# Kernel tuning notes

Measured on AMD Instinct MI355X. Metric: run time of the kernel, lower is better.

The kernel has to match this reference:

```python
import jax, jax.numpy as jnp
import numpy as np

B, N, D, H, DG = 1, 1024, 512, 8, 64
DK = D // H
EPS = 1e-5


def _layer_norm(x, g, b):
    m = jnp.mean(x, axis=-1, keepdims=True)
    v = jnp.var(x, axis=-1, keepdims=True)
    return (x - m) / jnp.sqrt(v + EPS) * g + b


def _box_rel_embedding(box):
    # box: (B, N, 4) = x_min, y_min, x_max, y_max
    x_min, y_min, x_max, y_max = [box[..., i] for i in range(4)]  # each (B, N)
    cx = (x_min + x_max) * 0.5
    cy = (y_min + y_max) * 0.5
    w = x_max - x_min + 1.0
    h = y_max - y_min + 1.0
    dx = jnp.log(jnp.clip(jnp.abs((cx[:, :, None] - cx[:, None, :]) / w[:, :, None]), 0.001))
    dy = jnp.log(jnp.clip(jnp.abs((cy[:, :, None] - cy[:, None, :]) / h[:, :, None]), 0.001))
    dw = jnp.log(w[:, :, None] / w[:, None, :])
    dh = jnp.log(h[:, :, None] / h[:, None, :])
    pos = jnp.stack([dx, dy, dw, dh], axis=-1)  # (B, N, N, 4)
    dim_mat = 1.0 / jnp.power(1000.0, jnp.arange(DG // 8, dtype=jnp.float32) / (DG // 8))  # (8,)
    mul = (100.0 * pos[..., None] * dim_mat).reshape(pos.shape[0], pos.shape[1], pos.shape[2], -1)  # (B,N,N,32)
    return jnp.concatenate([jnp.sin(mul), jnp.cos(mul)], axis=-1)  # (B, N, N, 64)


def _split_heads(x, W, b):
    # torch permute(2,0,1,3).view(-1, len, d_k): head-major flattening
    return (x @ W.T + b).reshape(B, N, H, DK).transpose(2, 0, 1, 3).reshape(H * B, N, DK)


def _forward(input_query, input_key, input_value, input_box,
             Wq, bq, Wk, bk, Wv, bv, Wo, bo, WG_w, WG_b,
             ln0_g, ln0_b, ln_g, ln_b):
    residual = input_query
    emb = _box_rel_embedding(input_box)  # (B, N, N, 64)
    # per-head linear (64 -> 1) then relu: (B, H, N, N)
    w_g = jax.nn.relu(jnp.einsum('bijg,hg->bhij', emb, WG_w) + WG_b[None, :, None, None])
    q = _split_heads(input_query, Wq, bq)  # (H*B, N, DK)
    k = _split_heads(input_key, Wk, bk)
    v = _split_heads(input_value, Wv, bv)
    scores = jnp.einsum('xnd,xmd->xnm', q, k) / np.sqrt(DK).astype(np.float32)  # (H*B, N, N)
    # original adds (B,H,N,N) to (H*B,N,N): only valid for B==1
    w_mn = jax.nn.softmax(jnp.log(jnp.clip(w_g.reshape(H * B, N, N), 1e-6)) + scores, axis=-1)
    x = jnp.einsum('xnm,xmd->xnd', w_mn, v)  # (H*B, N, DK)
    # faithful to original: transpose(1,2) then view(nbatches, -1, h*d_k)
    x = x.transpose(0, 2, 1).reshape(B, -1, H * DK)  # (B, N, D)
    out0 = _layer_norm(x + residual, ln0_g, ln0_b)
    out = out0 @ Wo.T + bo  # dropout = identity (eval mode)
    return _layer_norm(out + out0, ln_g, ln_b)


def setup_inputs() -> dict:
    key = jax.random.key(0)
    ks = jax.random.split(key, 12)
    inp = {}
    inp['input_query'] = jax.random.normal(ks[0], (B, N, D), dtype=jnp.float32)
    inp['input_key'] = jax.random.normal(ks[1], (B, N, D), dtype=jnp.float32)
    inp['input_value'] = jax.random.normal(ks[2], (B, N, D), dtype=jnp.float32)
    mins = jax.random.uniform(ks[3], (B, N, 2), dtype=jnp.float32) * 500.0
    sizes = jax.random.uniform(ks[4], (B, N, 2), dtype=jnp.float32) * 99.0 + 1.0
    inp['input_box'] = jnp.concatenate([mins, mins + sizes], axis=-1)  # valid boxes
    s = 0.02
    inp['Wq'] = jax.random.normal(ks[5], (D, D), dtype=jnp.float32) * s
    inp['bq'] = jnp.zeros((D,), dtype=jnp.float32)
    inp['Wk'] = jax.random.normal(ks[6], (D, D), dtype=jnp.float32) * s
    inp['bk'] = jnp.zeros((D,), dtype=jnp.float32)
    inp['Wv'] = jax.random.normal(ks[7], (D, D), dtype=jnp.float32) * s
    inp['bv'] = jnp.zeros((D,), dtype=jnp.float32)
    inp['Wo'] = jax.random.normal(ks[8], (D, D), dtype=jnp.float32) * s
    inp['bo'] = jnp.zeros((D,), dtype=jnp.float32)
    inp['WG_w'] = jax.random.normal(ks[9], (H, DG), dtype=jnp.float32) * 0.1
    inp['WG_b'] = jax.random.normal(ks[10], (H,), dtype=jnp.float32) * 0.1
    inp['ln0_g'] = jnp.ones((D,), dtype=jnp.float32)
    inp['ln0_b'] = jnp.zeros((D,), dtype=jnp.float32)
    inp['ln_g'] = jnp.ones((D,), dtype=jnp.float32)
    inp['ln_b'] = jnp.zeros((D,), dtype=jnp.float32)
    return inp


def reference(input_query, input_key, input_value, input_box,
              Wq, bq, Wk, bk, Wv, bv, Wo, bo, WG_w, WG_b,
              ln0_g, ln0_b, ln_g, ln_b):
    return _forward(input_query, input_key, input_value, input_box,
                    Wq, bq, Wk, bk, Wv, bv, Wo, bo, WG_w, WG_b,
                    ln0_g, ln0_b, ln_g, ln_b)
```

## Files before the change

### kernel.cpp

```cpp
#include <hip/hip_runtime.h>
#include <cstddef>

#define NTOK 1024
#define DMODEL 512
#define NHEAD 8
#define DKH 64
#define NSPLIT 4
#define JQ 256

typedef __attribute__((ext_vector_type(4))) float f32x4;
typedef __attribute__((ext_vector_type(8))) __bf16 bf16x8;
typedef __attribute__((ext_vector_type(4))) __bf16 bf16x4;
typedef __attribute__((ext_vector_type(4))) unsigned short u16x4;
typedef __attribute__((ext_vector_type(8))) unsigned short u16x8;
typedef __attribute__((ext_vector_type(4))) _Float16 f16x4;
typedef unsigned short ushort_t;

__device__ __forceinline__ float wave_sum_f(float v){
  #pragma unroll
  for (int m=1; m<64; m<<=1) v += __shfl_xor(v, m, 64);
  return v;
}
__device__ __forceinline__ unsigned short f2bf(float f){
  __bf16 b = (__bf16)f;
  return __builtin_bit_cast(unsigned short, b);
}
__device__ __forceinline__ float bf2f(unsigned short u){
  return (float)__builtin_bit_cast(__bf16, u);
}

__device__ __forceinline__ float fract_hw(float x){
  float r; asm("v_fract_f32 %0, %1" : "=v"(r) : "v"(x)); return r;
}
__device__ __forceinline__ float sin_rev(float rev){
  float f = fract_hw(rev);
  float s; asm("v_sin_f32 %0, %1" : "=v"(s) : "v"(f)); return s;
}
__device__ __forceinline__ float cos_rev(float rev){
  float f = fract_hw(rev);
  float c; asm("v_cos_f32 %0, %1" : "=v"(c) : "v"(f)); return c;
}
__device__ __forceinline__ float log_hw(float x){
  float l; asm("v_log_f32 %0, %1" : "=v"(l) : "v"(x));
  return 0.69314718056f * l;
}
__device__ __forceinline__ float exp_hw(float x){
  float y = x * 1.44269504f;
  float e; asm("v_exp_f32 %0, %1" : "=v"(e) : "v"(y));
  return e;
}

__global__ __launch_bounds__(256) void k_pre(
    const float* __restrict__ box, const float* __restrict__ WGw, const float* __restrict__ WGb,
    _Float16* __restrict__ wg16,
    const float* __restrict__ q, const float* __restrict__ k, const float* __restrict__ v,
    const float* __restrict__ wq, const float* __restrict__ wk, const float* __restrict__ wv,
    const float* __restrict__ wo,
    ushort_t* __restrict__ qb, ushort_t* __restrict__ kb, ushort_t* __restrict__ vb,
    ushort_t* __restrict__ wqb, ushort_t* __restrict__ wkb, ushort_t* __restrict__ wvb,
    ushort_t* __restrict__ wob){
  const int t = threadIdx.x;
  if (blockIdx.x >= 1024){
    int gi = (blockIdx.x - 1024)*256 + t;
    const float* s; ushort_t* d; int off;
    if (gi < 196608){
      int seg = gi >> 16;
      off = (gi & 65535)*8;
      s = seg==0 ? q : seg==1 ? k : v;
      d = seg==0 ? qb : seg==1 ? kb : vb;
    } else {
      int g2 = gi - 196608;
      int seg = g2 >> 15;
      off = (g2 & 32767)*8;
      s = seg==0 ? wq : seg==1 ? wk : seg==2 ? wv : wo;
      d = seg==0 ? wqb : seg==1 ? wkb : seg==2 ? wvb : wob;
    }
    float4 a = *(const float4*)(s + off);
    float4 b = *(const float4*)(s + off + 4);
    u16x4 o0, o1;
    o0[0]=f2bf(a.x); o0[1]=f2bf(a.y); o0[2]=f2bf(a.z); o0[3]=f2bf(a.w);
    o1[0]=f2bf(b.x); o1[1]=f2bf(b.y); o1[2]=f2bf(b.z); o1[3]=f2bf(b.w);
    *(u16x4*)(d + off) = o0;
    *(u16x4*)(d + off + 4) = o1;
    return;
  }
  __shared__ float arr[4][1024];
  #pragma unroll
  for (int u=0; u<4; u++){
    int idx = u*256 + t;
    float4 b4 = *(const float4*)(box + idx*4);
    arr[0][idx] = (b4.x + b4.z)*0.5f;
    arr[1][idx] = (b4.y + b4.w)*0.5f;
    arr[2][idx] = log_hw(b4.z - b4.x + 1.0f);
    arr[3][idx] = log_hw(b4.w - b4.y + 1.0f);
  }
  const int i = blockIdx.x;
  const int lane = t & 63, w = t >> 6, li = lane & 15, g = lane >> 4;
  float4 bi = *(const float4*)(box + i*4);
  float wi = bi.z - bi.x + 1.0f, hi = bi.w - bi.y + 1.0f;
  float Pi = (g==0) ? (bi.x+bi.z)*0.5f : (g==1) ? (bi.y+bi.w)*0.5f
           : (g==2) ? log_hw(wi) : log_hw(hi);
  float Ri = (g==0) ? 1.0f/wi : (g==1) ? 1.0f/hi : 1.0f;
  const bool doLog = (g < 2);
  bf16x8 wfs = {}, wfc = {};
  float wgb_li = 0.0f;
  if (li < 8){
    #pragma unroll
    for (int e=0; e<8; e++){
      wfs[e] = (__bf16)WGw[li*64 + g*8 + e];
      wfc[e] = (__bf16)WGw[li*64 + 32 + g*8 + e];
    }
    wgb_li = WGb[li];
  }
  __syncthreads();
  const float* parr = &arr[g][0];
  const float DMrev[8] = {15.9154943f, 6.7115094f, 2.8302196f, 1.1934938f,
                          0.5032921f, 0.2122365f, 0.08949941f, 0.0377416f};
  const int jbeg = w*256;
  for (int it=0; it<16; ++it){
    int j = jbeg + it*16 + li;
    float diff = (Pi - parr[j])*Ri;
    float lg = log_hw(fmaxf(fabsf(diff), 1e-3f));
    float dv = doLog ? lg : diff;
    bf16x8 afs, afc;
    #pragma unroll
    for (int e=0; e<8; e++){
      float rev = dv * DMrev[e];
      afs[e] = (__bf16)sin_rev(rev);
      afc[e] = (__bf16)cos_rev(rev);
    }
    f32x4 acc = (f32x4){0.f,0.f,0.f,0.f};
    acc = __builtin_amdgcn_mfma_f32_16x16x32_bf16(afs, wfs, acc, 0,0,0);
    acc = __builtin_amdgcn_mfma_f32_16x16x32_bf16(afc, wfc, acc, 0,0,0);
    if (li < 8){
      f16x4 o;
      #pragma unroll
      for (int r=0; r<4; r++)
        o[r] = (_Float16)fmaxf(acc[r] + wgb_li, 6.103515625e-05f);
      *(f16x4*)(wg16 + (((size_t)li<<20) + ((size_t)i<<10) + jbeg + it*16 + g*4)) = o;
    }
  }
}

__global__ __launch_bounds__(128) void k_mm_qkv(
    const ushort_t* __restrict__ Aq, const ushort_t* __restrict__ Ak, const ushort_t* __restrict__ Av,
    const ushort_t* __restrict__ Wqb, const ushort_t* __restrict__ Wkb, const ushort_t* __restrict__ Wvb,
    const float* __restrict__ bq, const float* __restrict__ bk, const float* __restrict__ bv,
    ushort_t* __restrict__ Qb, ushort_t* __restrict__ Kb, ushort_t* __restrict__ Vt){
  const int z = blockIdx.z;
  const ushort_t* A = z==0 ? Aq : z==1 ? Ak : Av;
  const ushort_t* W = z==0 ? Wqb : z==1 ? Wkb : Wvb;
  const float* bias = z==0 ? bq : z==1 ? bk : bv;
  const int t = threadIdx.x, lane = t & 63, w = t >> 6;
  const int li = lane & 15, g = lane >> 4;
  const int m0 = blockIdx.y*32;
  const int n0 = blockIdx.x*64 + w*32;
  const ushort_t* ar = A + (size_t)(m0+li)*DMODEL + g*8;
  const ushort_t* wr = W + (size_t)(n0+li)*DMODEL + g*8;
  f32x4 acc[2][2] = {};
  if (z < 2){
    #pragma unroll
    for (int k0=0; k0<DMODEL; k0+=64){
      bf16x8 wf0a = *(const bf16x8*)(wr + k0);
      bf16x8 wf0b = *(const bf16x8*)(wr + k0 + 32);
      bf16x8 wf1a = *(const bf16x8*)(wr + 16*DMODEL + k0);
      bf16x8 wf1b = *(const bf16x8*)(wr + 16*DMODEL + k0 + 32);
      bf16x8 af0a = *(const bf16x8*)(ar + k0);
      bf16x8 af0b = *(const bf16x8*)(ar + k0 + 32);
      bf16x8 af1a = *(const bf16x8*)(ar + 16*DMODEL + k0);
      bf16x8 af1b = *(const bf16x8*)(ar + 16*DMODEL + k0 + 32);
      acc[0][0] = __builtin_amdgcn_mfma_f32_16x16x32_bf16(wf0a, af0a, acc[0][0], 0,0,0);
      acc[0][0] = __builtin_amdgcn_mfma_f32_16x16x32_bf16(wf0b, af0b, acc[0][0], 0,0,0);
      acc[0][1] = __builtin_amdgcn_mfma_f32_16x16x32_bf16(wf0a, af1a, acc[0][1], 0,0,0);
      acc[0][1] = __builtin_amdgcn_mfma_f32_16x16x32_bf16(wf0b, af1b, acc[0][1], 0,0,0);
      acc[1][0] = __builtin_amdgcn_mfma_f32_16x16x32_bf16(wf1a, af0a, acc[1][0], 0,0,0);
      acc[1][0] = __builtin_amdgcn_mfma_f32_16x16x32_bf16(wf1b, af0b, acc[1][0], 0,0,0);
      acc[1][1] = __builtin_amdgcn_mfma_f32_16x16x32_bf16(wf1a, af1a, acc[1][1], 0,0,0);
      acc[1][1] = __builtin_amdgcn_mfma_f32_16x16x32_bf16(wf1b, af1b, acc[1][1], 0,0,0);
    }
    ushort_t* C = z ? Kb : Qb;
    #pragma unroll
    for (int nf=0; nf<2; nf++){
      int n = n0 + nf*16 + g*4;
      float4 b4 = *(const float4*)(bias + n);
      const float* bp = (const float*)&b4;
      #pragma unroll
      for (int mf=0; mf<2; mf++){
        int m = m0 + mf*16 + li;
        u16x4 o;
        #pragma unroll
        for (int r=0; r<4; r++) o[r] = f2bf(acc[nf][mf][r] + bp[r]);
        *(u16x4*)(C + (size_t)m*DMODEL + n) = o;
      }
    }
  } else {
    #pragma unroll
    for (int k0=0; k0<DMODEL; k0+=64){
      bf16x8 wf0a = *(const bf16x8*)(wr + k0);
      bf16x8 wf0b = *(const bf16x8*)(wr + k0 + 32);
      bf16x8 wf1a = *(const bf16x8*)(wr + 16*DMODEL + k0);
      bf16x8 wf1b = *(const bf16x8*)(wr + 16*DMODEL + k0 + 32);
      bf16x8 af0a = *(const bf16x8*)(ar + k0);
      bf16x8 af0b = *(const bf16x8*)(ar + k0 + 32);
      bf16x8 af1a = *(const bf16x8*)(ar + 16*DMODEL + k0);
      bf16x8 af1b = *(const bf16x8*)(ar + 16*DMODEL + k0 + 32);
      acc[0][0] = __builtin_amdgcn_mfma_f32_16x16x32_bf16(af0a, wf0a, acc[0][0], 0,0,0);
      acc[0][0] = __builtin_amdgcn_mfma_f32_16x16x32_bf16(af0b, wf0b, acc[0][0], 0,0,0);
      acc[0][1] = __builtin_amdgcn_mfma_f32_16x16x32_bf16(af0a, wf1a, acc[0][1], 0,0,0);
      acc[0][1] = __builtin_amdgcn_mfma_f32_16x16x32_bf16(af0b, wf1b, acc[0][1], 0,0,0);
      acc[1][0] = __builtin_amdgcn_mfma_f32_16x16x32_bf16(af1a, wf0a, acc[1][0], 0,0,0);
      acc[1][0] = __builtin_amdgcn_mfma_f32_16x16x32_bf16(af1b, wf0b, acc[1][0], 0,0,0);
      acc[1][1] = __builtin_amdgcn_mfma_f32_16x16x32_bf16(af1a, wf1a, acc[1][1], 0,0,0);
      acc[1][1] = __builtin_amdgcn_mfma_f32_16x16x32_bf16(af1b, wf1b, acc[1][1], 0,0,0);
    }
    #pragma unroll
    for (int mf=0; mf<2; mf++){
      int m = m0 + mf*16 + g*4;
      #pragma unroll
      for (int nf=0; nf<2; nf++){
        int n = n0 + nf*16 + li;
        float bn = bias[n];
        u16x4 o;
        #pragma unroll
        for (int r=0; r<4; r++) o[r] = f2bf(acc[mf][nf][r] + bn);
        *(u16x4*)(Vt + (((size_t)(n>>6))<<16) + ((size_t)(n&63)<<10) + m) = o;
      }
    }
  }
}

__global__ __launch_bounds__(512) void k_attn3(const ushort_t* __restrict__ Qb,
     const ushort_t* __restrict__ Kb, const ushort_t* __restrict__ Vt,
     const _Float16* __restrict__ wg, ushort_t* __restrict__ Xpt, float* __restrict__ rsp){
  __shared__ ushort_t Ks[256*68];
  __shared__ ushort_t Vs[64*264];
  const int t = threadIdx.x;
  const int itg = blockIdx.x, h = blockIdx.y, sp = blockIdx.z;
  const int jbeg = sp*JQ;
  {
    const int r = t >> 3, c = (t & 7)*8;
    #pragma unroll
    for (int p=0; p<4; p++){
      u16x8 kv = *(const u16x8*)(Kb + (size_t)(jbeg + p*64 + r)*DMODEL + h*DKH + c);
      *(u16x8*)(Ks + (p*64 + r)*68 + c) = kv;
      u16x8 vv = *(const u16x8*)(Vt + ((size_t)h<<16) + (size_t)r*NTOK + jbeg + p*64 + c);
      *(u16x8*)(Vs + r*264 + p*64 + c) = vv;
    }
  }
  const int lane = t & 63, w = t >> 6;
  const int i0 = (itg*8 + w)*16;
  const int li = lane & 15, g = lane >> 4;
  const ushort_t* qp = Qb + (size_t)(i0+li)*DMODEL + h*DKH + g*8;
  bf16x8 qf0 = *(const bf16x8*)(qp);
  bf16x8 qf1 = *(const bf16x8*)(qp + 32);
  const _Float16* gbase = wg + ((size_t)h<<20) + ((size_t)(i0+li)<<10) + jbeg + g*4;
  f32x4 xacc[4];
  #pragma unroll
  for (int mf=0; mf<4; mf++) xacc[mf] = (f32x4){0.f,0.f,0.f,0.f};
  float rsum = 0.f;
  __syncthreads();
  #pragma unroll
  for (int jj = 0; jj < JQ; jj += 32){
    const ushort_t* kp = Ks + (jj + li)*68 + g*8;
    bf16x8 a00 = *(const bf16x8*)(kp);
    bf16x8 a01 = *(const bf16x8*)(kp + 32);
    bf16x8 a10 = *(const bf16x8*)(kp + 16*68);
    bf16x8 a11 = *(const bf16x8*)(kp + 16*68 + 32);
    f32x4 s0 = (f32x4){0.f,0.f,0.f,0.f};
    f32x4 s1 = (f32x4){0.f,0.f,0.f,0.f};
    s0 = __builtin_amdgcn_mfma_f32_16x16x32_bf16(a00, qf0, s0, 0,0,0);
    s0 = __builtin_amdgcn_mfma_f32_16x16x32_bf16(a01, qf1, s0, 0,0,0);
    s1 = __builtin_amdgcn_mfma_f32_16x16x32_bf16(a10, qf0, s1, 0,0,0);
    s1 = __builtin_amdgcn_mfma_f32_16x16x32_bf16(a11, qf1, s1, 0,0,0);
    f16x4 g0 = *(const f16x4*)(gbase + jj);
    f16x4 g1 = *(const f16x4*)(gbase + jj + 16);
    float p[8];
    #pragma unroll
    for (int r=0; r<4; r++){ p[r]   = (float)g0[r] * exp_hw(s0[r]*0.125f); rsum += p[r]; }
    #pragma unroll
    for (int r=0; r<4; r++){ p[4+r] = (float)g1[r] * exp_hw(s1[r]*0.125f); rsum += p[4+r]; }
    bf16x8 pb;
    pb[0]=(__bf16)p[0]; pb[1]=(__bf16)p[1]; pb[2]=(__bf16)p[2]; pb[3]=(__bf16)p[3];
    pb[4]=(__bf16)p[4]; pb[5]=(__bf16)p[5]; pb[6]=(__bf16)p[6]; pb[7]=(__bf16)p[7];
    #pragma unroll
    for (int mf=0; mf<4; mf++){
      const ushort_t* vp = Vs + (size_t)(li + mf*16)*264 + jj + g*4;
      bf16x4 lo = *(const bf16x4*)(vp);
      bf16x4 hi = *(const bf16x4*)(vp + 16);
      bf16x8 vf = __builtin_shufflevector(lo, hi, 0,1,2,3,4,5,6,7);
      xacc[mf] = __builtin_amdgcn_mfma_f32_16x16x32_bf16(vf, pb, xacc[mf], 0,0,0);
    }
  }
  rsum += __shfl_xor(rsum, 16, 64);
  rsum += __shfl_xor(rsum, 32, 64);
  if (lane < 16) rsp[((size_t)sp*NHEAD + h)*NTOK + i0 + li] = rsum;
  __syncthreads();
  float* xw = (float*)Ks + w*(16*68);
  #pragma unroll
  for (int mf=0; mf<4; mf++)
    *(f32x4*)&xw[li*68 + mf*16 + g*4] = xacc[mf];
  __builtin_amdgcn_s_waitcnt(0);
  float xv[16];
  #pragma unroll
  for (int r=0; r<16; r++) xv[r] = xw[r*68 + lane];
  u16x8 o0, o1;
  #pragma unroll
  for (int r=0; r<8; r++){ o0[r] = f2bf(xv[r]); o1[r] = f2bf(xv[8+r]); }
  ushort_t* xp = Xpt + (((size_t)sp*NHEAD + h)*DKH + lane)*NTOK + i0;
  *(u16x8*)(xp)     = o0;
  *(u16x8*)(xp + 8) = o1;
}

__global__ __launch_bounds__(256) void k_ln0c(const ushort_t* __restrict__ Xpt,
        const float* __restrict__ rsp, const float* __restrict__ resid,
        const float* __restrict__ g, const float* __restrict__ b,
        float* __restrict__ out0, ushort_t* __restrict__ out0b){
  const int n = blockIdx.x, t = threadIdx.x;
  const int h = n >> 7, dk = (n >> 1) & 63, mo = (n & 1)*512;
  const int i0 = mo + t, i1 = mo + t + 256;
  float s0v=0.f, s1v=0.f, r0=0.f, r1=0.f;
  #pragma unroll
  for (int sp=0; sp<NSPLIT; sp++){
    const ushort_t* base = Xpt + (((size_t)sp*NHEAD + h)*DKH + dk)*NTOK;
    s0v += bf2f(base[i0]);
    s1v += bf2f(base[i1]);
    const float* rb = rsp + ((size_t)sp*NHEAD + h)*NTOK;
    r0 += rb[i0];
    r1 += rb[i1];
  }
  float x0 = s0v/r0 + resid[(size_t)n*DMODEL + t];
  float x1 = s1v/r1 + resid[(size_t)n*DMODEL + t + 256];
  __shared__ float red[8];
  float s = wave_sum_f(x0 + x1);
  float q = wave_sum_f(x0*x0 + x1*x1);
  int wid = t >> 6, lane = t & 63;
  if (lane == 0){ red[wid] = s; red[4+wid] = q; }
  __syncthreads();
  float S = red[0]+red[1]+red[2]+red[3];
  float Q = red[4]+red[5]+red[6]+red[7];
  float mean = S * (1.0f/512.0f);
  float var = Q * (1.0f/512.0f) - mean*mean;
  float rs = rsqrtf(var + 1e-5f);
  float y0 = (x0-mean)*rs*g[t] + b[t];
  float y1 = (x1-mean)*rs*g[t+256] + b[t+256];
  out0[(size_t)n*DMODEL + t]        = y0;
  out0[(size_t)n*DMODEL + t + 256]  = y1;
  out0b[(size_t)n*DMODEL + t]       = f2bf(y0);
  out0b[(size_t)n*DMODEL + t + 256] = f2bf(y1);
}

__global__ __launch_bounds__(512) void k_mm_o_ln(
    const ushort_t* __restrict__ A, const ushort_t* __restrict__ W,
    const float* __restrict__ bo, const float* __restrict__ add,
    const float* __restrict__ lng, const float* __restrict__ lnb, float* __restrict__ out){
  const int t = threadIdx.x, lane = t & 63, w = t >> 6;
  const int li = lane & 15, g = lane >> 4;
  const int m0 = blockIdx.x*16;
  const int n0 = w*64;
  const ushort_t* ar = A + (size_t)(m0+li)*DMODEL + g*8;
  const ushort_t* wr = W + (size_t)(n0+li)*DMODEL + g*8;
  f32x4 acc[4] = {};
  #pragma unroll
  for (int k0=0; k0<DMODEL; k0+=64){
    bf16x8 afa = *(const bf16x8*)(ar + k0);
    bf16x8 afb = *(const bf16x8*)(ar + k0 + 32);
    #pragma unroll
    for (int nf=0; nf<4; nf++){
      const ushort_t* wp = wr + (size_t)nf*16*DMODEL + k0;
      bf16x8 wfa = *(const bf16x8*)(wp);
      bf16x8 wfb = *(const bf16x8*)(wp + 32);
      acc[nf] = __builtin_amdgcn_mfma_f32_16x16x32_bf16(wfa, afa, acc[nf], 0,0,0);
      acc[nf] = __builtin_amdgcn_mfma_f32_16x16x32_bf16(wfb, afb, acc[nf], 0,0,0);
    }
  }
  const int m = m0 + li;
  float s = 0.f, qq = 0.f;
  f32x4 v[4];
  #pragma unroll
  for (int nf=0; nf<4; nf++){
    int n = n0 + nf*16 + g*4;
    f32x4 b4 = *(const f32x4*)(bo + n);
    f32x4 a4 = *(const f32x4*)(add + (size_t)m*DMODEL + n);
    #pragma unroll
    for (int r=0; r<4; r++){
      float x = acc[nf][r] + b4[r] + a4[r];
      v[nf][r] = x; s += x; qq += x*x;
    }
  }
  s  += __shfl_xor(s, 16, 64);  s  += __shfl_xor(s, 32, 64);
  qq += __shfl_xor(qq, 16, 64); qq += __shfl_xor(qq, 32, 64);
  __shared__ float red[8][16][2];
  if (g == 0){ red[w][li][0] = s; red[w][li][1] = qq; }
  __syncthreads();
  float S = 0.f, Q = 0.f;
  #pragma unroll
  for (int u=0; u<8; u++){ S += red[u][li][0]; Q += red[u][li][1]; }
  float mean = S * (1.0f/512.0f);
  float var = Q * (1.0f/512.0f) - mean*mean;
  float rs = rsqrtf(var + 1e-5f);
  #pragma unroll
  for (int nf=0; nf<4; nf++){
    int n = n0 + nf*16 + g*4;
    f32x4 g4 = *(const f32x4*)(lng + n);
    f32x4 be = *(const f32x4*)(lnb + n);
    f32x4 o;
    #pragma unroll
    for (int r=0; r<4; r++) o[r] = (v[nf][r]-mean)*rs*g4[r] + be[r];
    *(f32x4*)(out + (size_t)m*DMODEL + n) = o;
  }
}

extern "C" void kernel_launch(void* const* d_in, const int* in_sizes, int n_in,
                              void* d_out, int out_size, void* d_ws, size_t ws_size,
                              hipStream_t stream){
  (void)in_sizes; (void)n_in; (void)out_size; (void)ws_size;
  const float* in_q = (const float*)d_in[0];
  const float* in_k = (const float*)d_in[1];
  const float* in_v = (const float*)d_in[2];
  const float* box  = (const float*)d_in[3];
  const float* Wq   = (const float*)d_in[4];
  const float* bq   = (const float*)d_in[5];
  const float* Wk   = (const float*)d_in[6];
  const float* bk   = (const float*)d_in[7];
  const float* Wv   = (const float*)d_in[8];
  const float* bv   = (const float*)d_in[9];
  const float* Wo   = (const float*)d_in[10];
  const float* bo   = (const float*)d_in[11];
  const float* WGw  = (const float*)d_in[12];
  const float* WGb  = (const float*)d_in[13];
  const float* ln0g = (const float*)d_in[14];
  const float* ln0b = (const float*)d_in[15];
  const float* lng  = (const float*)d_in[16];
  const float* lnb  = (const float*)d_in[17];

  float* ws = (float*)d_ws;
  ushort_t* Abq  = (ushort_t*)(ws + 0);
  ushort_t* Abk  = (ushort_t*)(ws + 262144);
  ushort_t* Abv  = (ushort_t*)(ws + 524288);
  ushort_t* Wqb  = (ushort_t*)(ws + 786432);
  ushort_t* Wkb  = (ushort_t*)(ws + 917504);
  ushort_t* Wvb  = (ushort_t*)(ws + 1048576);
  ushort_t* Wob  = (ushort_t*)(ws + 1179648);
  ushort_t* Qb   = (ushort_t*)(ws + 1310720);
  ushort_t* Kb   = (ushort_t*)(ws + 1572864);
  ushort_t* Vt   = (ushort_t*)(ws + 1835008);
  _Float16* wg16 = (_Float16*)(ws + 2097152);
  ushort_t* Xpt  = (ushort_t*)(ws + 6291456);
  float*    rsp  = ws + 8388608;
  float*    out0 = ws + 8421376;
  ushort_t* out0b= (ushort_t*)(ws + 8945664);
  float*    out  = (float*)d_out;

  k_pre<<<dim3(2304), dim3(256), 0, stream>>>(box, WGw, WGb, wg16,
            in_q, in_k, in_v, Wq, Wk, Wv, Wo,
            Abq, Abk, Abv, Wqb, Wkb, Wvb, Wob);
  k_mm_qkv<<<dim3(8,32,3), dim3(128), 0, stream>>>(Abq, Abk, Abv, Wqb, Wkb, Wvb,
            bq, bk, bv, Qb, Kb, Vt);
  k_attn3<<<dim3(8,8,4), dim3(512), 0, stream>>>(Qb, Kb, Vt, wg16, Xpt, rsp);
  k_ln0c<<<dim3(1024), dim3(256), 0, stream>>>(Xpt, rsp, in_q, ln0g, ln0b, out0, out0b);
  k_mm_o_ln<<<dim3(64), dim3(512), 0, stream>>>(out0b, Wob, bo, out0, lng, lnb, out);
}
```

Measured before the change: 77.92 us.

## Fuse all five stages into one persistent kernel with grid-wide barriers

Replaces the five separate launches (preprocessing, QKV projection, attention, LayerNorm-combine, output projection with LayerNorm) with one persistent kernel of 256 blocks of 512 threads. A software grid barrier built on global atomics separates the stages, and the barrier counter is reset with a memset before each launch. The aim is to remove per-launch overhead and the gaps between kernels. In exchange, every stage now runs on a fixed 256-block grid whose work distribution differs from the original tuned grids. The barrier also relies on all blocks being co-resident, so it can deadlock or add spin cost if they are not.

After: 222.7 us. 2.86x slower.

```diff
diff --git a/kernel.cpp b/kernel.cpp
--- a/kernel.cpp
+++ b/kernel.cpp
@@ -50,363 +50,385 @@
   return e;
 }
 
-__global__ __launch_bounds__(256) void k_pre(
+__device__ __forceinline__ void gsync(unsigned* bar){
+  __syncthreads();
+  if (threadIdx.x == 0){
+    unsigned gen = __hip_atomic_load(bar+1, __ATOMIC_RELAXED, __HIP_MEMORY_SCOPE_AGENT);
+    unsigned prev = __hip_atomic_fetch_add(bar, 1u, __ATOMIC_ACQ_REL, __HIP_MEMORY_SCOPE_AGENT);
+    if (prev == 255u){
+      __hip_atomic_store(bar, 0u, __ATOMIC_RELAXED, __HIP_MEMORY_SCOPE_AGENT);
+      __hip_atomic_store(bar+1, gen+1u, __ATOMIC_RELEASE, __HIP_MEMORY_SCOPE_AGENT);
+    } else {
+      while (__hip_atomic_load(bar+1, __ATOMIC_ACQUIRE, __HIP_MEMORY_SCOPE_AGENT) == gen)
+        __builtin_amdgcn_s_sleep(2);
+    }
+  }
+  __syncthreads();
+}
+
+__global__ __launch_bounds__(512) void k_mega(
     const float* __restrict__ box, const float* __restrict__ WGw, const float* __restrict__ WGb,
     _Float16* __restrict__ wg16,
-    const float* __restrict__ q, const float* __restrict__ k, const float* __restrict__ v,
-    const float* __restrict__ wq, const float* __restrict__ wk, const float* __restrict__ wv,
-    const float* __restrict__ wo,
-    ushort_t* __restrict__ qb, ushort_t* __restrict__ kb, ushort_t* __restrict__ vb,
-    ushort_t* __restrict__ wqb, ushort_t* __restrict__ wkb, ushort_t* __restrict__ wvb,
-    ushort_t* __restrict__ wob){
+    const float* __restrict__ inq, const float* __restrict__ ink, const float* __restrict__ inv,
+    const float* __restrict__ Wq, const float* __restrict__ Wk, const float* __restrict__ Wv,
+    const float* __restrict__ Wo,
+    ushort_t* __restrict__ Abq, ushort_t* __restrict__ Abk, ushort_t* __restrict__ Abv,
+    ushort_t* __restrict__ Wqb, ushort_t* __restrict__ Wkb, ushort_t* __restrict__ Wvb,
+    ushort_t* __restrict__ Wob,
+    const float* __restrict__ bq, const float* __restrict__ bk, const float* __restrict__ bv,
+    ushort_t* __restrict__ Qb, ushort_t* __restrict__ Kb, ushort_t* __restrict__ Vt,
+    ushort_t* __restrict__ Xpt, float* __restrict__ rsp,
+    const float* __restrict__ ln0g, const float* __restrict__ ln0b,
+    float* __restrict__ out0, ushort_t* __restrict__ out0b,
+    const float* __restrict__ bo, const float* __restrict__ lng, const float* __restrict__ lnb,
+    float* __restrict__ out, unsigned* bar){
+  __shared__ __align__(16) char smem[68608];
   const int t = threadIdx.x;
-  if (blockIdx.x >= 1024){
-    int gi = (blockIdx.x - 1024)*256 + t;
-    const float* s; ushort_t* d; int off;
-    if (gi < 196608){
-      int seg = gi >> 16;
-      off = (gi & 65535)*8;
-      s = seg==0 ? q : seg==1 ? k : v;
-      d = seg==0 ? qb : seg==1 ? kb : vb;
+  const int b = blockIdx.x;
+  const int lane = t & 63, w = t >> 6;
+  const int li = lane & 15, g = lane >> 4;
+  const int wid = b*8 + w;
+
+  {
+    float* arr = (float*)smem;
+    #pragma unroll
+    for (int u=0; u<2; u++){
+      int idx = u*512 + t;
+      float4 b4 = *(const float4*)(box + idx*4);
+      arr[idx]      = (b4.x + b4.z)*0.5f;
+      arr[1024+idx] = (b4.y + b4.w)*0.5f;
+      arr[2048+idx] = log_hw(b4.z - b4.x + 1.0f);
+      arr[3072+idx] = log_hw(b4.w - b4.y + 1.0f);
+    }
+    __syncthreads();
+    bf16x8 wfs = {}, wfc = {};
+    float wgb_li = 0.0f;
+    if (li < 8){
+      #pragma unroll
+      for (int e=0; e<8; e++){
+        wfs[e] = (__bf16)WGw[li*64 + g*8 + e];
+        wfc[e] = (__bf16)WGw[li*64 + 32 + g*8 + e];
+      }
+      wgb_li = WGb[li];
+    }
+    const float* parr = arr + g*1024;
+    const float DMrev[8] = {15.9154943f, 6.7115094f, 2.8302196f, 1.1934938f,
+                            0.5032921f, 0.2122365f, 0.08949941f, 0.0377416f};
+    #pragma unroll
+    for (int pass=0; pass<2; pass++){
+      const int unit = wid + pass*2048;
+      const int i = unit >> 2;
+      const int jbeg = (unit & 3)*256;
+      float4 bi = *(const float4*)(box + i*4);
+      float wi_ = bi.z - bi.x + 1.0f, hi_ = bi.w - bi.y + 1.0f;
+      float Pi = (g==0) ? (bi.x+bi.z)*0.5f : (g==1) ? (bi.y+bi.w)*0.5f
+               : (g==2) ? log_hw(wi_) : log_hw(hi_);
+      float Ri = (g==0) ? 1.0f/wi_ : (g==1) ? 1.0f/hi_ : 1.0f;
+      const bool doLog = (g < 2);
+      for (int it=0; it<16; ++it){
+        int j = jbeg + it*16 + li;
+        float diff = (Pi - parr[j])*Ri;
+        float lg = log_hw(fmaxf(fabsf(diff), 1e-3f));
+        float dv = doLog ? lg : diff;
+        bf16x8 afs, afc;
+        #pragma unroll
+        for (int e=0; e<8; e++){
+          float rev = dv * DMrev[e];
+          afs[e] = (__bf16)sin_rev(rev);
+          afc[e] = (__bf16)cos_rev(rev);
+        }
+        f32x4 acc = (f32x4){0.f,0.f,0.f,0.f};
+        acc = __builtin_amdgcn_mfma_f32_16x16x32_bf16(afs, wfs, acc, 0,0,0);
+        acc = __builtin_amdgcn_mfma_f32_16x16x32_bf16(afc, wfc, acc, 0,0,0);
+        if (li < 8){
+          f16x4 o;
+          #pragma unroll
+          for (int r=0; r<4; r++)
+            o[r] = (_Float16)fmaxf(acc[r] + wgb_li, 6.103515625e-05f);
+          *(f16x4*)(wg16 + (((size_t)li<<20) + ((size_t)i<<10) + jbeg + it*16 + g*4)) = o;
+        }
+      }
+    }
+    #pragma unroll
+    for (int kk=0; kk<3; kk++){
+      int gi = b*512 + t + kk*131072;
+      if (gi < 327680){
+        const float* s; ushort_t* d; int off;
+        if (gi < 196608){
+          int seg = gi >> 16;
+          off = (gi & 65535)*8;
+          s = seg==0 ? inq : seg==1 ? ink : inv;
+          d = seg==0 ? Abq : seg==1 ? Abk : Abv;
+        } else {
+          int g2 = gi - 196608;
+          int seg = g2 >> 15;
+          off = (g2 & 32767)*8;
+          s = seg==0 ? Wq : seg==1 ? Wk : seg==2 ? Wv : Wo;
+          d = seg==0 ? Wqb : seg==1 ? Wkb : seg==2 ? Wvb : Wob;
+        }
+        float4 a = *(const float4*)(s + off);
+        float4 b4 = *(const float4*)(s + off + 4);
+        u16x4 o0, o1;
+        o0[0]=f2bf(a.x); o0[1]=f2bf(a.y); o0[2]=f2bf(a.z); o0[3]=f2bf(a.w);
+        o1[0]=f2bf(b4.x); o1[1]=f2bf(b4.y); o1[2]=f2bf(b4.z); o1[3]=f2bf(b4.w);
+        *(u16x4*)(d + off) = o0;
+        *(u16x4*)(d + off + 4) = o1;
+      }
+    }
+  }
+  gsync(bar);
+
+  if (wid < 1536){
+    const int z = wid / 512;
+    const int rem = wid - z*512;
+    const int my = rem >> 4;
+    const int nx = (rem & 15) >> 1;
+    const int w2 = rem & 1;
+    const int m0 = my*32;
+    const int n0 = nx*64 + w2*32;
+    const ushort_t* A = z==0 ? Abq : z==1 ? Abk : Abv;
+    const ushort_t* W = z==0 ? Wqb : z==1 ? Wkb : Wvb;
+    const float* bias = z==0 ? bq : z==1 ? bk : bv;
+    const ushort_t* ar = A + (size_t)(m0+li)*DMODEL + g*8;
+    const ushort_t* wr = W + (size_t)(n0+li)*DMODEL + g*8;
+    f32x4 acc[2][2] = {};
+    if (z < 2){
+      #pragma unroll
+      for (int k0=0; k0<DMODEL; k0+=64){
+        bf16x8 wf0a = *(const bf16x8*)(wr + k0);
+        bf16x8 wf0b = *(const bf16x8*)(wr + k0 + 32);
+        bf16x8 wf1a = *(const bf16x8*)(wr + 16*DMODEL + k0);
+        bf16x8 wf1b = *(const bf16x8*)(wr + 16*DMODEL + k0 + 32);
+        bf16x8 af0a = *(const bf16x8*)(ar + k0);
+        bf16x8 af0b = *(const bf16x8*)(ar + k0 + 32);
+        bf16x8 af1a = *(const bf16x8*)(ar + 16*DMODEL + k0);
+        bf16x8 af1b = *(const bf16x8*)(ar + 16*DMODEL + k0 + 32);
+        acc[0][0] = __builtin_amdgcn_mfma_f32_16x16x32_bf16(wf0a, af0a, acc[0][0], 0,0,0);
+        acc[0][0] = __builtin_amdgcn_mfma_f32_16x16x32_bf16(wf0b, af0b, acc[0][0], 0,0,0);
+        acc[0][1] = __builtin_amdgcn_mfma_f32_16x16x32_bf16(wf0a, af1a, acc[0][1], 0,0,0);
+        acc[0][1] = __builtin_amdgcn_mfma_f32_16x16x32_bf16(wf0b, af1b, acc[0][1], 0,0,0);
+        acc[1][0] = __builtin_amdgcn_mfma_f32_16x16x32_bf16(wf1a, af0a, acc[1][0], 0,0,0);
+        acc[1][0] = __builtin_amdgcn_mfma_f32_16x16x32_bf16(wf1b, af0b, acc[1][0], 0,0,0);
+        acc[1][1] = __builtin_amdgcn_mfma_f32_16x16x32_bf16(wf1a, af1a, acc[1][1], 0,0,0);
+        acc[1][1] = __builtin_amdgcn_mfma_f32_16x16x32_bf16(wf1b, af1b, acc[1][1], 0,0,0);
+      }
+      ushort_t* C = z ? Kb : Qb;
+      #pragma unroll
+      for (int nf=0; nf<2; nf++){
+        int n = n0 + nf*16 + g*4;
+        float4 b4 = *(const float4*)(bias + n);
+        const float* bp = (const float*)&b4;
+        #pragma unroll
+        for (int mf=0; mf<2; mf++){
+          int m = m0 + mf*16 + li;
+          u16x4 o;
+          #pragma unroll
+          for (int r=0; r<4; r++) o[r] = f2bf(acc[nf][mf][r] + bp[r]);
+          *(u16x4*)(C + (size_t)m*DMODEL + n) = o;
+        }
+      }
     } else {
-      int g2 = gi - 196608;
-      int seg = g2 >> 15;
-      off = (g2 & 32767)*8;
-      s = seg==0 ? wq : seg==1 ? wk : seg==2 ? wv : wo;
-      d = seg==0 ? wqb : seg==1 ? wkb : seg==2 ? wvb : wob;
-    }
-    float4 a = *(const float4*)(s + off);
-    float4 b = *(const float4*)(s + off + 4);
-    u16x4 o0, o1;
-    o0[0]=f2bf(a.x); o0[1]=f2bf(a.y); o0[2]=f2bf(a.z); o0[3]=f2bf(a.w);
-    o1[0]=f2bf(b.x); o1[1]=f2bf(b.y); o1[2]=f2bf(b.z); o1[3]=f2bf(b.w);
-    *(u16x4*)(d + off) = o0;
-    *(u16x4*)(d + off + 4) = o1;
-    return;
-  }
-  __shared__ float arr[4][1024];
-  #pragma unroll
-  for (int u=0; u<4; u++){
-    int idx = u*256 + t;
-    float4 b4 = *(const float4*)(box + idx*4);
-    arr[0][idx] = (b4.x + b4.z)*0.5f;
-    arr[1][idx] = (b4.y + b4.w)*0.5f;
-    arr[2][idx] = log_hw(b4.z - b4.x + 1.0f);
-    arr[3][idx] = log_hw(b4.w - b4.y + 1.0f);
-  }
-  const int i = blockIdx.x;
-  const int lane = t & 63, w = t >> 6, li = lane & 15, g = lane >> 4;
-  float4 bi = *(const float4*)(box + i*4);
-  float wi = bi.z - bi.x + 1.0f, hi = bi.w - bi.y + 1.0f;
-  float Pi = (g==0) ? (bi.x+bi.z)*0.5f : (g==1) ? (bi.y+bi.w)*0.5f
-           : (g==2) ? log_hw(wi) : log_hw(hi);
-  float Ri = (g==0) ? 1.0f/wi : (g==1) ? 1.0f/hi : 1.0f;
-  const bool doLog = (g < 2);
-  bf16x8 wfs = {}, wfc = {};
-  float wgb_li = 0.0f;
-  if (li < 8){
-    #pragma unroll
-    for (int e=0; e<8; e++){
-      wfs[e] = (__bf16)WGw[li*64 + g*8 + e];
-      wfc[e] = (__bf16)WGw[li*64 + 32 + g*8 + e];
-    }
-    wgb_li = WGb[li];
-  }
-  __syncthreads();
-  const float* parr = &arr[g][0];
-  const float DMrev[8] = {15.9154943f, 6.7115094f, 2.8302196f, 1.1934938f,
-                          0.5032921f, 0.2122365f, 0.08949941f, 0.0377416f};
-  const int jbeg = w*256;
-  for (int it=0; it<16; ++it){
-    int j = jbeg + it*16 + li;
-    float diff = (Pi - parr[j])*Ri;
-    float lg = log_hw(fmaxf(fabsf(diff), 1e-3f));
-    float dv = doLog ? lg : diff;
-    bf16x8 afs, afc;
-    #pragma unroll
-    for (int e=0; e<8; e++){
-      float rev = dv * DMrev[e];
-      afs[e] = (__bf16)sin_rev(rev);
-      afc[e] = (__bf16)cos_rev(rev);
-    }
-    f32x4 acc = (f32x4){0.f,0.f,0.f,0.f};
-    acc = __builtin_amdgcn_mfma_f32_16x16x32_bf16(afs, wfs, acc, 0,0,0);
-    acc = __builtin_amdgcn_mfma_f32_16x16x32_bf16(afc, wfc, acc, 0,0,0);
-    if (li < 8){
-      f16x4 o;
-      #pragma unroll
-      for (int r=0; r<4; r++)
-        o[r] = (_Float16)fmaxf(acc[r] + wgb_li, 6.103515625e-05f);
-      *(f16x4*)(wg16 + (((size_t)li<<20) + ((size_t)i<<10) + jbeg + it*16 + g*4)) = o;
-    }
-  }
-}
-
-__global__ __launch_bounds__(128) void k_mm_qkv(
-    const ushort_t* __restrict__ Aq, const ushort_t* __restrict__ Ak, const ushort_t* __restrict__ Av,
-    const ushort_t* __restrict__ Wqb, const ushort_t* __restrict__ Wkb, const ushort_t* __restrict__ Wvb,
-    const float* __restrict__ bq, const float* __restrict__ bk, const float* __restrict__ bv,
-    ushort_t* __restrict__ Qb, ushort_t* __restrict__ Kb, ushort_t* __restrict__ Vt){
-  const int z = blockIdx.z;
-  const ushort_t* A = z==0 ? Aq : z==1 ? Ak : Av;
-  const ushort_t* W = z==0 ? Wqb : z==1 ? Wkb : Wvb;
-  const float* bias = z==0 ? bq : z==1 ? bk : bv;
-  const int t = threadIdx.x, lane = t & 63, w = t >> 6;
-  const int li = lane & 15, g = lane >> 4;
-  const int m0 = blockIdx.y*32;
-  const int n0 = blockIdx.x*64 + w*32;
-  const ushort_t* ar = A + (size_t)(m0+li)*DMODEL + g*8;
-  const ushort_t* wr = W + (size_t)(n0+li)*DMODEL + g*8;
-  f32x4 acc[2][2] = {};
-  if (z < 2){
+      #pragma unroll
+      for (int k0=0; k0<DMODEL; k0+=64){
+        bf16x8 wf0a = *(const bf16x8*)(wr + k0);
+        bf16x8 wf0b = *(const bf16x8*)(wr + k0 + 32);
+        bf16x8 wf1a = *(const bf16x8*)(wr + 16*DMODEL + k0);
+        bf16x8 wf1b = *(const bf16x8*)(wr + 16*DMODEL + k0 + 32);
+        bf16x8 af0a = *(const bf16x8*)(ar + k0);
+        bf16x8 af0b = *(const bf16x8*)(ar + k0 + 32);
+        bf16x8 af1a = *(const bf16x8*)(ar + 16*DMODEL + k0);
+        bf16x8 af1b = *(const bf16x8*)(ar + 16*DMODEL + k0 + 32);
+        acc[0][0] = __builtin_amdgcn_mfma_f32_16x16x32_bf16(af0a, wf0a, acc[0][0], 0,0,0);
+        acc[0][0] = __builtin_amdgcn_mfma_f32_16x16x32_bf16(af0b, wf0b, acc[0][0], 0,0,0);
+        acc[0][1] = __builtin_amdgcn_mfma_f32_16x16x32_bf16(af0a, wf1a, acc[0][1], 0,0,0);
+        acc[0][1] = __builtin_amdgcn_mfma_f32_16x16x32_bf16(af0b, wf1b, acc[0][1], 0,0,0);
+        acc[1][0] = __builtin_amdgcn_mfma_f32_16x16x32_bf16(af1a, wf0a, acc[1][0], 0,0,0);
+        acc[1][0] = __builtin_amdgcn_mfma_f32_16x16x32_bf16(af1b, wf0b, acc[1][0], 0,0,0);
+        acc[1][1] = __builtin_amdgcn_mfma_f32_16x16x32_bf16(af1a, wf1a, acc[1][1], 0,0,0);
+        acc[1][1] = __builtin_amdgcn_mfma_f32_16x16x32_bf16(af1b, wf1b, acc[1][1], 0,0,0);
+      }
+      #pragma unroll
+      for (int mf=0; mf<2; mf++){
+        int m = m0 + mf*16 + g*4;
+        #pragma unroll
+        for (int nf=0; nf<2; nf++){
+          int n = n0 + nf*16 + li;
+          float bn = bias[n];
+          u16x4 o;
+          #pragma unroll
+          for (int r=0; r<4; r++) o[r] = f2bf(acc[mf][nf][r] + bn);
+          *(u16x4*)(Vt + (((size_t)(n>>6))<<16) + ((size_t)(n&63)<<10) + m) = o;
+        }
+      }
+    }
+  }
+  gsync(bar);
+
+  {
+    const int itg = b & 7, h = (b>>3) & 7, sp = b >> 6;
+    const int jbeg = sp*JQ;
+    ushort_t* Ks = (ushort_t*)smem;
+    ushort_t* Vs = (ushort_t*)(smem + 34816);
+    {
+      const int r = t >> 3, c = (t & 7)*8;
+      #pragma unroll
+      for (int p=0; p<4; p++){
+        u16x8 kv = *(const u16x8*)(Kb + (size_t)(jbeg + p*64 + r)*DMODEL + h*DKH + c);
+        *(u16x8*)(Ks + (p*64 + r)*68 + c) = kv;
+        u16x8 vv = *(const u16x8*)(Vt + ((size_t)h<<16) + (size_t)r*NTOK + jbeg + p*64 + c);
+        *(u16x8*)(Vs + r*264 + p*64 + c) = vv;
+      }
+    }
+    const int i0 = (itg*8 + w)*16;
+    const ushort_t* qp = Qb + (size_t)(i0+li)*DMODEL + h*DKH + g*8;
+    bf16x8 qf0 = *(const bf16x8*)(qp);
+    bf16x8 qf1 = *(const bf16x8*)(qp + 32);
+    const _Float16* gbase = wg16 + ((size_t)h<<20) + ((size_t)(i0+li)<<10) + jbeg + g*4;
+    f32x4 xacc[4];
+    #pragma unroll
+    for (int mf=0; mf<4; mf++) xacc[mf] = (f32x4){0.f,0.f,0.f,0.f};
+    float rsum = 0.f;
+    __syncthreads();
+    #pragma unroll
+    for (int jj = 0; jj < JQ; jj += 32){
+      const ushort_t* kp = Ks + (jj + li)*68 + g*8;
+      bf16x8 a00 = *(const bf16x8*)(kp);
+      bf16x8 a01 = *(const bf16x8*)(kp + 32);
+      bf16x8 a10 = *(const bf16x8*)(kp + 16*68);
+      bf16x8 a11 = *(const bf16x8*)(kp + 16*68 + 32);
+      f32x4 s0 = (f32x4){0.f,0.f,0.f,0.f};
+      f32x4 s1 = (f32x4){0.f,0.f,0.f,0.f};
+      s0 = __builtin_amdgcn_mfma_f32_16x16x32_bf16(a00, qf0, s0, 0,0,0);
+      s0 = __builtin_amdgcn_mfma_f32_16x16x32_bf16(a01, qf1, s0, 0,0,0);
+      s1 = __builtin_amdgcn_mfma_f32_16x16x32_bf16(a10, qf0, s1, 0,0,0);
+      s1 = __builtin_amdgcn_mfma_f32_16x16x32_bf16(a11, qf1, s1, 0,0,0);
+      f16x4 g0 = *(const f16x4*)(gbase + jj);
+      f16x4 g1 = *(const f16x4*)(gbase + jj + 16);
+      float p[8];
+      #pragma unroll
+      for (int r=0; r<4; r++){ p[r]   = (float)g0[r] * exp_hw(s0[r]*0.125f); rsum += p[r]; }
+      #pragma unroll
+      for (int r=0; r<4; r++){ p[4+r] = (float)g1[r] * exp_hw(s1[r]*0.125f); rsum += p[4+r]; }
+      bf16x8 pb;
+      pb[0]=(__bf16)p[0]; pb[1]=(__bf16)p[1]; pb[2]=(__bf16)p[2]; pb[3]=(__bf16)p[3];
+      pb[4]=(__bf16)p[4]; pb[5]=(__bf16)p[5]; pb[6]=(__bf16)p[6]; pb[7]=(__bf16)p[7];
+      #pragma unroll
+      for (int mf=0; mf<4; mf++){
+        const ushort_t* vp = Vs + (size_t)(li + mf*16)*264 + jj + g*4;
+        bf16x4 lo = *(const bf16x4*)(vp);
+        bf16x4 hi = *(const bf16x4*)(vp + 16);
+        bf16x8 vf = __builtin_shufflevector(lo, hi, 0,1,2,3,4,5,6,7);
+        xacc[mf] = __builtin_amdgcn_mfma_f32_16x16x32_bf16(vf, pb, xacc[mf], 0,0,0);
+      }
+    }
+    rsum += __shfl_xor(rsum, 16, 64);
+    rsum += __shfl_xor(rsum, 32, 64);
+    if (lane < 16) rsp[((size_t)sp*NHEAD + h)*NTOK + i0 + li] = rsum;
+    __syncthreads();
+    float* xw = (float*)Ks + w*(16*68);
+    #pragma unroll
+    for (int mf=0; mf<4; mf++)
+      *(f32x4*)&xw[li*68 + mf*16 + g*4] = xacc[mf];
+    __builtin_amdgcn_s_waitcnt(0);
+    float xv[16];
+    #pragma unroll
+    for (int r=0; r<16; r++) xv[r] = xw[r*68 + lane];
+    u16x8 o0, o1;
+    #pragma unroll
+    for (int r=0; r<8; r++){ o0[r] = f2bf(xv[r]); o1[r] = f2bf(xv[8+r]); }
+    ushort_t* xp = Xpt + (((size_t)sp*NHEAD + h)*DKH + lane)*NTOK + i0;
+    *(u16x8*)(xp)     = o0;
+    *(u16x8*)(xp + 8) = o1;
+  }
+  gsync(bar);
+
+  if (wid < 1024){
+    const int n = wid;
+    const int h = n >> 7, dk = (n >> 1) & 63, mo = (n & 1)*512;
+    float x[8];
+    float sum = 0.f, sq = 0.f;
+    #pragma unroll
+    for (int c=0; c<8; c++){
+      int d = c*64 + lane;
+      int i = mo + d;
+      float sv = 0.f, rv = 0.f;
+      #pragma unroll
+      for (int sp=0; sp<NSPLIT; sp++){
+        sv += bf2f(Xpt[(((size_t)sp*NHEAD + h)*DKH + dk)*NTOK + i]);
+        rv += rsp[((size_t)sp*NHEAD + h)*NTOK + i];
+      }
+      x[c] = sv/rv + inq[(size_t)n*DMODEL + d];
+      sum += x[c]; sq += x[c]*x[c];
+    }
+    sum = wave_sum_f(sum);
+    sq  = wave_sum_f(sq);
+    float mean = sum * (1.0f/512.0f);
+    float var = sq * (1.0f/512.0f) - mean*mean;
+    float rs = rsqrtf(var + 1e-5f);
+    #pragma unroll
+    for (int c=0; c<8; c++){
+      int d = c*64 + lane;
+      float y = (x[c]-mean)*rs*ln0g[d] + ln0b[d];
+      out0[(size_t)n*DMODEL + d]  = y;
+      out0b[(size_t)n*DMODEL + d] = f2bf(y);
+    }
+  }
+  gsync(bar);
+
+  if (b < 64){
+    float (*red)[16][2] = (float(*)[16][2])smem;
+    const int m0 = b*16;
+    const int n0 = w*64;
+    const ushort_t* ar = out0b + (size_t)(m0+li)*DMODEL + g*8;
+    const ushort_t* wr = Wob + (size_t)(n0+li)*DMODEL + g*8;
+    f32x4 acc[4] = {};
     #pragma unroll
     for (int k0=0; k0<DMODEL; k0+=64){
-      bf16x8 wf0a = *(const bf16x8*)(wr + k0);
-      bf16x8 wf0b = *(const bf16x8*)(wr + k0 + 32);
-      bf16x8 wf1a = *(const bf16x8*)(wr + 16*DMODEL + k0);
-      bf16x8 wf1b = *(const bf16x8*)(wr + 16*DMODEL + k0 + 32);
-      bf16x8 af0a = *(const bf16x8*)(ar + k0);
-      bf16x8 af0b = *(const bf16x8*)(ar + k0 + 32);
-      bf16x8 af1a = *(const bf16x8*)(ar + 16*DMODEL + k0);
-      bf16x8 af1b = *(const bf16x8*)(ar + 16*DMODEL + k0 + 32);
-      acc[0][0] = __builtin_amdgcn_mfma_f32_16x16x32_bf16(wf0a, af0a, acc[0][0], 0,0,0);
-      acc[0][0] = __builtin_amdgcn_mfma_f32_16x16x32_bf16(wf0b, af0b, acc[0][0], 0,0,0);
-      acc[0][1] = __builtin_amdgcn_mfma_f32_16x16x32_bf16(wf0a, af1a, acc[0][1], 0,0,0);
-      acc[0][1] = __builtin_amdgcn_mfma_f32_16x16x32_bf16(wf0b, af1b, acc[0][1], 0,0,0);
-      acc[1][0] = __builtin_amdgcn_mfma_f32_16x16x32_bf16(wf1a, af0a, acc[1][0], 0,0,0);
-      acc[1][0] = __builtin_amdgcn_mfma_f32_16x16x32_bf16(wf1b, af0b, acc[1][0], 0,0,0);
-      acc[1][1] = __builtin_amdgcn_mfma_f32_16x16x32_bf16(wf1a, af1a, acc[1][1], 0,0,0);
-      acc[1][1] = __builtin_amdgcn_mfma_f32_16x16x32_bf16(wf1b, af1b, acc[1][1], 0,0,0);
-    }
-    ushort_t* C = z ? Kb : Qb;
-    #pragma unroll
-    for (int nf=0; nf<2; nf++){
+      bf16x8 afa = *(const bf16x8*)(ar + k0);
+      bf16x8 afb = *(const bf16x8*)(ar + k0 + 32);
+      #pragma unroll
+      for (int nf=0; nf<4; nf++){
+        const ushort_t* wp = wr + (size_t)nf*16*DMODEL + k0;
+        bf16x8 wfa = *(const bf16x8*)(wp);
+        bf16x8 wfb = *(const bf16x8*)(wp + 32);
+        acc[nf] = __builtin_amdgcn_mfma_f32_16x16x32_bf16(wfa, afa, acc[nf], 0,0,0);
+        acc[nf] = __builtin_amdgcn_mfma_f32_16x16x32_bf16(wfb, afb, acc[nf], 0,0,0);
+      }
+    }
+    const int m = m0 + li;
+    float s = 0.f, qq = 0.f;
+    f32x4 v[4];
+    #pragma unroll
+    for (int nf=0; nf<4; nf++){
       int n = n0 + nf*16 + g*4;
-      float4 b4 = *(const float4*)(bias + n);
-      const float* bp = (const float*)&b4;
-      #pragma unroll
-      for (int mf=0; mf<2; mf++){
-        int m = m0 + mf*16 + li;
-        u16x4 o;
-        #pragma unroll
-        for (int r=0; r<4; r++) o[r] = f2bf(acc[nf][mf][r] + bp[r]);
-        *(u16x4*)(C + (size_t)m*DMODEL + n) = o;
-      }
-    }
-  } else {
-    #pragma unroll
-    for (int k0=0; k0<DMODEL; k0+=64){
-      bf16x8 wf0a = *(const bf16x8*)(wr + k0);
-      bf16x8 wf0b = *(const bf16x8*)(wr + k0 + 32);
-      bf16x8 wf1a = *(const bf16x8*)(wr + 16*DMODEL + k0);
-      bf16x8 wf1b = *(const bf16x8*)(wr + 16*DMODEL + k0 + 32);
-      bf16x8 af0a = *(const bf16x8*)(ar + k0);
-      bf16x8 af0b = *(const bf16x8*)(ar + k0 + 32);
-      bf16x8 af1a = *(const bf16x8*)(ar + 16*DMODEL + k0);
-      bf16x8 af1b = *(const bf16x8*)(ar + 16*DMODEL + k0 + 32);
-      acc[0][0] = __builtin_amdgcn_mfma_f32_16x16x32_bf16(af0a, wf0a, acc[0][0], 0,0,0);
-      acc[0][0] = __builtin_amdgcn_mfma_f32_16x16x32_bf16(af0b, wf0b, acc[0][0], 0,0,0);
-      acc[0][1] = __builtin_amdgcn_mfma_f32_16x16x32_bf16(af0a, wf1a, acc[0][1], 0,0,0);
-      acc[0][1] = __builtin_amdgcn_mfma_f32_16x16x32_bf16(af0b, wf1b, acc[0][1], 0,0,0);
-      acc[1][0] = __builtin_amdgcn_mfma_f32_16x16x32_bf16(af1a, wf0a, acc[1][0], 0,0,0);
-      acc[1][0] = __builtin_amdgcn_mfma_f32_16x16x32_bf16(af1b, wf0b, acc[1][0], 0,0,0);
-      acc[1][1] = __builtin_amdgcn_mfma_f32_16x16x32_bf16(af1a, wf1a, acc[1][1], 0,0,0);
-      acc[1][1] = __builtin_amdgcn_mfma_f32_16x16x32_bf16(af1b, wf1b, acc[1][1], 0,0,0);
-    }
-    #pragma unroll
-    for (int mf=0; mf<2; mf++){
-      int m = m0 + mf*16 + g*4;
-      #pragma unroll
-      for (int nf=0; nf<2; nf++){
-        int n = n0 + nf*16 + li;
-        float bn = bias[n];
-        u16x4 o;
-        #pragma unroll
-        for (int r=0; r<4; r++) o[r] = f2bf(acc[mf][nf][r] + bn);
-        *(u16x4*)(Vt + (((size_t)(n>>6))<<16) + ((size_t)(n&63)<<10) + m) = o;
-      }
-    }
-  }
-}
-
-__global__ __launch_bounds__(512) void k_attn3(const ushort_t* __restrict__ Qb,
-     const ushort_t* __restrict__ Kb, const ushort_t* __restrict__ Vt,
-     const _Float16* __restrict__ wg, ushort_t* __restrict__ Xpt, float* __restrict__ rsp){
-  __shared__ ushort_t Ks[256*68];
-  __shared__ ushort_t Vs[64*264];
-  const int t = threadIdx.x;
-  const int itg = blockIdx.x, h = blockIdx.y, sp = blockIdx.z;
-  const int jbeg = sp*JQ;
-  {
-    const int r = t >> 3, c = (t & 7)*8;
-    #pragma unroll
-    for (int p=0; p<4; p++){
-      u16x8 kv = *(const u16x8*)(Kb + (size_t)(jbeg + p*64 + r)*DMODEL + h*DKH + c);
-      *(u16x8*)(Ks + (p*64 + r)*68 + c) = kv;
-      u16x8 vv = *(const u16x8*)(Vt + ((size_t)h<<16) + (size_t)r*NTOK + jbeg + p*64 + c);
-      *(u16x8*)(Vs + r*264 + p*64 + c) = vv;
-    }
-  }
-  const int lane = t & 63, w = t >> 6;
-  const int i0 = (itg*8 + w)*16;
-  const int li = lane & 15, g = lane >> 4;
-  const ushort_t* qp = Qb + (size_t)(i0+li)*DMODEL + h*DKH + g*8;
-  bf16x8 qf0 = *(const bf16x8*)(qp);
-  bf16x8 qf1 = *(const bf16x8*)(qp + 32);
-  const _Float16* gbase = wg + ((size_t)h<<20) + ((size_t)(i0+li)<<10) + jbeg + g*4;
-  f32x4 xacc[4];
-  #pragma unroll
-  for (int mf=0; mf<4; mf++) xacc[mf] = (f32x4){0.f,0.f,0.f,0.f};
-  float rsum = 0.f;
-  __syncthreads();
-  #pragma unroll
-  for (int jj = 0; jj < JQ; jj += 32){
-    const ushort_t* kp = Ks + (jj + li)*68 + g*8;
-    bf16x8 a00 = *(const bf16x8*)(kp);
-    bf16x8 a01 = *(const bf16x8*)(kp + 32);
-    bf16x8 a10 = *(const bf16x8*)(kp + 16*68);
-    bf16x8 a11 = *(const bf16x8*)(kp + 16*68 + 32);
-    f32x4 s0 = (f32x4){0.f,0.f,0.f,0.f};
-    f32x4 s1 = (f32x4){0.f,0.f,0.f,0.f};
-    s0 = __builtin_amdgcn_mfma_f32_16x16x32_bf16(a00, qf0, s0, 0,0,0);
-    s0 = __builtin_amdgcn_mfma_f32_16x16x32_bf16(a01, qf1, s0, 0,0,0);
-    s1 = __builtin_amdgcn_mfma_f32_16x16x32_bf16(a10, qf0, s1, 0,0,0);
-    s1 = __builtin_amdgcn_mfma_f32_16x16x32_bf16(a11, qf1, s1, 0,0,0);
-    f16x4 g0 = *(const f16x4*)(gbase + jj);
-    f16x4 g1 = *(const f16x4*)(gbase + jj + 16);
-    float p[8];
-    #pragma unroll
-    for (int r=0; r<4; r++){ p[r]   = (float)g0[r] * exp_hw(s0[r]*0.125f); rsum += p[r]; }
-    #pragma unroll
-    for (int r=0; r<4; r++){ p[4+r] = (float)g1[r] * exp_hw(s1[r]*0.125f); rsum += p[4+r]; }
-    bf16x8 pb;
-    pb[0]=(__bf16)p[0]; pb[1]=(__bf16)p[1]; pb[2]=(__bf16)p[2]; pb[3]=(__bf16)p[3];
-    pb[4]=(__bf16)p[4]; pb[5]=(__bf16)p[5]; pb[6]=(__bf16)p[6]; pb[7]=(__bf16)p[7];
-    #pragma unroll
-    for (int mf=0; mf<4; mf++){
-      const ushort_t* vp = Vs + (size_t)(li + mf*16)*264 + jj + g*4;
-      bf16x4 lo = *(const bf16x4*)(vp);
-      bf16x4 hi = *(const bf16x4*)(vp + 16);
-      bf16x8 vf = __builtin_shufflevector(lo, hi, 0,1,2,3,4,5,6,7);
-      xacc[mf] = __builtin_amdgcn_mfma_f32_16x16x32_bf16(vf, pb, xacc[mf], 0,0,0);
-    }
-  }
-  rsum += __shfl_xor(rsum, 16, 64);
-  rsum += __shfl_xor(rsum, 32, 64);
-  if (lane < 16) rsp[((size_t)sp*NHEAD + h)*NTOK + i0 + li] = rsum;
-  __syncthreads();
-  float* xw = (float*)Ks + w*(16*68);
-  #pragma unroll
-  for (int mf=0; mf<4; mf++)
-    *(f32x4*)&xw[li*68 + mf*16 + g*4] = xacc[mf];
-  __builtin_amdgcn_s_waitcnt(0);
-  float xv[16];
-  #pragma unroll
-  for (int r=0; r<16; r++) xv[r] = xw[r*68 + lane];
-  u16x8 o0, o1;
-  #pragma unroll
-  for (int r=0; r<8; r++){ o0[r] = f2bf(xv[r]); o1[r] = f2bf(xv[8+r]); }
-  ushort_t* xp = Xpt + (((size_t)sp*NHEAD + h)*DKH + lane)*NTOK + i0;
-  *(u16x8*)(xp)     = o0;
-  *(u16x8*)(xp + 8) = o1;
-}
-
-__global__ __launch_bounds__(256) void k_ln0c(const ushort_t* __restrict__ Xpt,
-        const float* __restrict__ rsp, const float* __restrict__ resid,
-        const float* __restrict__ g, const float* __restrict__ b,
-        float* __restrict__ out0, ushort_t* __restrict__ out0b){
-  const int n = blockIdx.x, t = threadIdx.x;
-  const int h = n >> 7, dk = (n >> 1) & 63, mo = (n & 1)*512;
-  const int i0 = mo + t, i1 = mo + t + 256;
-  float s0v=0.f, s1v=0.f, r0=0.f, r1=0.f;
-  #pragma unroll
-  for (int sp=0; sp<NSPLIT; sp++){
-    const ushort_t* base = Xpt + (((size_t)sp*NHEAD + h)*DKH + dk)*NTOK;
-    s0v += bf2f(base[i0]);
-    s1v += bf2f(base[i1]);
-    const float* rb = rsp + ((size_t)sp*NHEAD + h)*NTOK;
-    r0 += rb[i0];
-    r1 += rb[i1];
-  }
-  float x0 = s0v/r0 + resid[(size_t)n*DMODEL + t];
-  float x1 = s1v/r1 + resid[(size_t)n*DMODEL + t + 256];
-  __shared__ float red[8];
-  float s = wave_sum_f(x0 + x1);
-  float q = wave_sum_f(x0*x0 + x1*x1);
-  int wid = t >> 6, lane = t & 63;
-  if (lane == 0){ red[wid] = s; red[4+wid] = q; }
-  __syncthreads();
-  float S = red[0]+red[1]+red[2]+red[3];
-  float Q = red[4]+red[5]+red[6]+red[7];
-  float mean = S * (1.0f/512.0f);
-  float var = Q * (1.0f/512.0f) - mean*mean;
-  float rs = rsqrtf(var + 1e-5f);
-  float y0 = (x0-mean)*rs*g[t] + b[t];
-  float y1 = (x1-mean)*rs*g[t+256] + b[t+256];
-  out0[(size_t)n*DMODEL + t]        = y0;
-  out0[(size_t)n*DMODEL + t + 256]  = y1;
-  out0b[(size_t)n*DMODEL + t]       = f2bf(y0);
-  out0b[(size_t)n*DMODEL + t + 256] = f2bf(y1);
-}
-
-__global__ __launch_bounds__(512) void k_mm_o_ln(
-    const ushort_t* __restrict__ A, const ushort_t* __restrict__ W,
-    const float* __restrict__ bo, const float* __restrict__ add,
-    const float* __restrict__ lng, const float* __restrict__ lnb, float* __restrict__ out){
-  const int t = threadIdx.x, lane = t & 63, w = t >> 6;
-  const int li = lane & 15, g = lane >> 4;
-  const int m0 = blockIdx.x*16;
-  const int n0 = w*64;
-  const ushort_t* ar = A + (size_t)(m0+li)*DMODEL + g*8;
-  const ushort_t* wr = W + (size_t)(n0+li)*DMODEL + g*8;
-  f32x4 acc[4] = {};
-  #pragma unroll
-  for (int k0=0; k0<DMODEL; k0+=64){
-    bf16x8 afa = *(const bf16x8*)(ar + k0);
-    bf16x8 afb = *(const bf16x8*)(ar + k0 + 32);
+      f32x4 b4 = *(const f32x4*)(bo + n);
+      f32x4 a4 = *(const f32x4*)(out0 + (size_t)m*DMODEL + n);
+      #pragma unroll
+      for (int r=0; r<4; r++){
+        float x = acc[nf][r] + b4[r] + a4[r];
+        v[nf][r] = x; s += x; qq += x*x;
+      }
+    }
+    s  += __shfl_xor(s, 16, 64);  s  += __shfl_xor(s, 32, 64);
+    qq += __shfl_xor(qq, 16, 64); qq += __shfl_xor(qq, 32, 64);
+    if (g == 0){ red[w][li][0] = s; red[w][li][1] = qq; }
+    __syncthreads();
+    float S = 0.f, Q = 0.f;
+    #pragma unroll
+    for (int u=0; u<8; u++){ S += red[u][li][0]; Q += red[u][li][1]; }
+    float mean = S * (1.0f/512.0f);
+    float var = Q * (1.0f/512.0f) - mean*mean;
+    float rs = rsqrtf(var + 1e-5f);
     #pragma unroll
     for (int nf=0; nf<4; nf++){
-      const ushort_t* wp = wr + (size_t)nf*16*DMODEL + k0;
-      bf16x8 wfa = *(const bf16x8*)(wp);
-      bf16x8 wfb = *(const bf16x8*)(wp + 32);
-      acc[nf] = __builtin_amdgcn_mfma_f32_16x16x32_bf16(wfa, afa, acc[nf], 0,0,0);
-      acc[nf] = __builtin_amdgcn_mfma_f32_16x16x32_bf16(wfb, afb, acc[nf], 0,0,0);
-    }
-  }
-  const int m = m0 + li;
-  float s = 0.f, qq = 0.f;
-  f32x4 v[4];
-  #pragma unroll
-  for (int nf=0; nf<4; nf++){
-    int n = n0 + nf*16 + g*4;
-    f32x4 b4 = *(const f32x4*)(bo + n);
-    f32x4 a4 = *(const f32x4*)(add + (size_t)m*DMODEL + n);
-    #pragma unroll
-    for (int r=0; r<4; r++){
-      float x = acc[nf][r] + b4[r] + a4[r];
-      v[nf][r] = x; s += x; qq += x*x;
-    }
-  }
-  s  += __shfl_xor(s, 16, 64);  s  += __shfl_xor(s, 32, 64);
-  qq += __shfl_xor(qq, 16, 64); qq += __shfl_xor(qq, 32, 64);
-  __shared__ float red[8][16][2];
-  if (g == 0){ red[w][li][0] = s; red[w][li][1] = qq; }
-  __syncthreads();
-  float S = 0.f, Q = 0.f;
-  #pragma unroll
-  for (int u=0; u<8; u++){ S += red[u][li][0]; Q += red[u][li][1]; }
-  float mean = S * (1.0f/512.0f);
-  float var = Q * (1.0f/512.0f) - mean*mean;
-  float rs = rsqrtf(var + 1e-5f);
-  #pragma unroll
-  for (int nf=0; nf<4; nf++){
-    int n = n0 + nf*16 + g*4;
-    f32x4 g4 = *(const f32x4*)(lng + n);
-    f32x4 be = *(const f32x4*)(lnb + n);
-    f32x4 o;
-    #pragma unroll
-    for (int r=0; r<4; r++) o[r] = (v[nf][r]-mean)*rs*g4[r] + be[r];
-    *(f32x4*)(out + (size_t)m*DMODEL + n) = o;
+      int n = n0 + nf*16 + g*4;
+      f32x4 g4 = *(const f32x4*)(lng + n);
+      f32x4 be = *(const f32x4*)(lnb + n);
+      f32x4 o;
+      #pragma unroll
+      for (int r=0; r<4; r++) o[r] = (v[nf][r]-mean)*rs*g4[r] + be[r];
+      *(f32x4*)(out + (size_t)m*DMODEL + n) = o;
+    }
   }
 }
 
@@ -449,14 +471,15 @@
   float*    rsp  = ws + 8388608;
   float*    out0 = ws + 8421376;
   ushort_t* out0b= (ushort_t*)(ws + 8945664);
+  unsigned* bar  = (unsigned*)(ws + 9437184);
   float*    out  = (float*)d_out;
 
-  k_pre<<<dim3(2304), dim3(256), 0, stream>>>(box, WGw, WGb, wg16,
-            in_q, in_k, in_v, Wq, Wk, Wv, Wo,
-            Abq, Abk, Abv, Wqb, Wkb, Wvb, Wob);
-  k_mm_qkv<<<dim3(8,32,3), dim3(128), 0, stream>>>(Abq, Abk, Abv, Wqb, Wkb, Wvb,
-            bq, bk, bv, Qb, Kb, Vt);
-  k_attn3<<<dim3(8,8,4), dim3(512), 0, stream>>>(Qb, Kb, Vt, wg16, Xpt, rsp);
-  k_ln0c<<<dim3(1024), dim3(256), 0, stream>>>(Xpt, rsp, in_q, ln0g, ln0b, out0, out0b);
-  k_mm_o_ln<<<dim3(64), dim3(512), 0, stream>>>(out0b, Wob, bo, out0, lng, lnb, out);
-}
+  hipMemsetAsync(bar, 0, 16, stream);
+  k_mega<<<dim3(256), dim3(512), 0, stream>>>(
+      box, WGw, WGb, wg16,
+      in_q, in_k, in_v, Wq, Wk, Wv, Wo,
+      Abq, Abk, Abv, Wqb, Wkb, Wvb, Wob,
+      bq, bk, bv, Qb, Kb, Vt, Xpt, rsp,
+      ln0g, ln0b, out0, out0b,
+      bo, lng, lnb, out, bar);
+}
```
